# Kernel tuning notes

Hardware: AMD Instinct MI355X
Metric: run time of the kernel (lower is better)

## Reference

```python
import jax, jax.numpy as jnp
import numpy as np

B, T, IN, H, P = 1024, 100, 1, 256, 0.5


def _lstm_scan(xs, h0, c0, Wih, Whh, bih, bhh, mask_h, mask_in=None):
    """Run an LSTMCell over time with variational dropout masks.
    xs: [T, B, D]. mask_h multiplies the recurrent hidden state (as in the
    original: cell(x_t, (h * mask1, c))); mask_in (optional) multiplies input.
    PyTorch LSTMCell gate order: i, f, g, o."""
    b = bih + bhh

    def step(carry, xt):
        h, c = carry
        xin = xt if mask_in is None else xt * mask_in
        g = xin @ Wih.T + (h * mask_h) @ Whh.T + b  # [B, 4H]
        i, f, gg, o = jnp.split(g, 4, axis=-1)
        c = jax.nn.sigmoid(f) * c + jax.nn.sigmoid(i) * jnp.tanh(gg)
        h = jax.nn.sigmoid(o) * jnp.tanh(c)
        return (h, c), h

    _, hs = jax.lax.scan(step, (h0, c0), xs)
    return hs  # [T, B, H]


def setup_inputs() -> dict:
    key = jax.random.key(0)
    ks = jax.random.split(key, 24)
    s = 1.0 / np.sqrt(H)

    def u(k, shape):
        return jax.random.uniform(k, shape, jnp.float32, -s, s)

    inp = {"x0": jax.random.normal(ks[0], (B, T, IN), jnp.float32)}
    names = ["1f", "1b", "2f", "2b"]
    in_sizes = [2 * IN, 2 * IN, 2 * H, 2 * H]
    i = 1
    for n, d in zip(names, in_sizes):
        inp[f"Wih{n}"] = u(ks[i], (4 * H, d)); i += 1
        inp[f"Whh{n}"] = u(ks[i], (4 * H, H)); i += 1
        inp[f"bih{n}"] = u(ks[i], (4 * H,)); i += 1
        inp[f"bhh{n}"] = u(ks[i], (4 * H,)); i += 1
    inp["Wout"] = u(ks[17], (IN, 2 * H))
    inp["bout"] = u(ks[18], (IN,))
    # Variational dropout masks (Bernoulli(1 - dropout_prob)), per set_dropout(batch)
    def bern(k, shape):
        return (jax.random.uniform(k, shape) > P).astype(jnp.float32)
    inp["mask1"] = bern(ks[19], (B, H))
    inp["mask2"] = bern(ks[20], (B, 2 * H))
    inp["mask3"] = bern(ks[21], (B, H))
    inp["mask4"] = bern(ks[22], (B, 1, 2 * H))
    return inp


def reference(x0,
              Wih1f, Whh1f, bih1f, bhh1f,
              Wih1b, Whh1b, bih1b, bhh1b,
              Wih2f, Whh2f, bih2f, bhh2f,
              Wih2b, Whh2b, bih2b, bhh2b,
              Wout, bout, mask1, mask2, mask3, mask4):
    batch = x0.shape[0]
    m = x0.mean(axis=1, keepdims=True)                       # [B, 1, IN]
    x = jnp.concatenate([x0 - m, jnp.broadcast_to(m, x0.shape)], axis=2)  # [B, T, 2*IN]
    xs = jnp.swapaxes(x, 0, 1)                               # [T, B, 2*IN]

    h0 = jnp.zeros((batch, H), x0.dtype)
    c0 = jnp.zeros((batch, H), x0.dtype)

    # Layer 1, forward and backward in time (backward outputs NOT re-flipped,
    # faithful to the original which stacks them in reversed-visit order).
    hf = _lstm_scan(xs, h0, c0, Wih1f, Whh1f, bih1f, bhh1f, mask1)
    hb = _lstm_scan(xs[::-1], h0, c0, Wih1b, Whh1b, bih1b, bhh1b, mask1)
    p1 = jnp.concatenate([hf, hb], axis=-1)                  # [T, B, 2H]

    # Layer 2 with input mask2 and recurrent mask3
    h2f = _lstm_scan(p1, h0, c0, Wih2f, Whh2f, bih2f, bhh2f, mask3, mask_in=mask2)
    h2b = _lstm_scan(p1[::-1], h0, c0, Wih2b, Whh2b, bih2b, bhh2b, mask3, mask_in=mask2)
    p2 = jnp.concatenate([h2f, h2b], axis=-1)                # [T, B, 2H]

    pa = jnp.swapaxes(p2, 0, 1)                              # [B, T, 2H]
    pred = (pa * mask4) @ Wout.T + bout                      # [B, T, IN]
    return pred + m
```

## Files before the change

kernel.cpp:

```cpp
#include <hip/hip_runtime.h>
#include <cstdint>
#include <cstddef>

#define B_  1024
#define T_  100
#define H_  256

typedef _Float16 f16x8 __attribute__((ext_vector_type(8)));
typedef float    f32x16 __attribute__((ext_vector_type(16)));

__device__ __forceinline__ float sigm(float x){ return 1.0f/(1.0f + __expf(-x)); }
__device__ __forceinline__ float tanh_(float x){ return 1.0f - 2.0f/(1.0f + __expf(2.0f*x)); }

#define W_WHH1F 0
#define W_WHH1B 262144
#define W_WIH2F 524288
#define W_WIH2B 1048576
#define W_WHH2F 1572864
#define W_WHH2B 1835008
#define W_TOTAL 2097152

__global__ void pack_weights(const float* __restrict__ Whh1f, const float* __restrict__ Whh1b,
                             const float* __restrict__ Wih2f, const float* __restrict__ Wih2b,
                             const float* __restrict__ Whh2f, const float* __restrict__ Whh2b,
                             _Float16* __restrict__ dst)
{
  int fid = blockIdx.x*256 + threadIdx.x;
  const float* src; int base, nkk, ksh, lf;
  if      (fid <  32768){ src=Whh1f; base=W_WHH1F; nkk=16; ksh=4; lf=fid; }
  else if (fid <  65536){ src=Whh1b; base=W_WHH1B; nkk=16; ksh=4; lf=fid-32768; }
  else if (fid < 131072){ src=Wih2f; base=W_WIH2F; nkk=32; ksh=5; lf=fid-65536; }
  else if (fid < 196608){ src=Wih2b; base=W_WIH2B; nkk=32; ksh=5; lf=fid-131072; }
  else if (fid < 229376){ src=Whh2f; base=W_WHH2F; nkk=16; ksh=4; lf=fid-196608; }
  else                  { src=Whh2b; base=W_WHH2B; nkk=16; ksh=4; lf=fid-229376; }
  int l  = lf & 63;
  int t  = lf >> 6;
  int kk = t & (nkk-1);
  int r  = t >> ksh;
  int g  = r & 3, cc = r >> 2;
  int K  = nkk*16;
  int n  = g*256 + cc*32 + (l & 31);
  int k  = kk*16 + ((l >> 5) << 3);
  const float4* s4 = (const float4*)(src + (size_t)n*K + k);
  float4 v0 = s4[0], v1 = s4[1];
  f16x8 o;
  o[0]=(_Float16)v0.x; o[1]=(_Float16)v0.y; o[2]=(_Float16)v0.z; o[3]=(_Float16)v0.w;
  o[4]=(_Float16)v1.x; o[5]=(_Float16)v1.y; o[6]=(_Float16)v1.z; o[7]=(_Float16)v1.w;
  *(f16x8*)(dst + (size_t)base + (size_t)lf*8) = o;
}

__global__ __launch_bounds__(512, 2)
void l1_phase(const _Float16* __restrict__ wpool,
              const float* __restrict__ Wih_f, const float* __restrict__ Wih_b,
              const float* __restrict__ bih_f, const float* __restrict__ bhh_f,
              const float* __restrict__ bih_b, const float* __restrict__ bhh_b,
              const float* __restrict__ x0, const float* __restrict__ mvec,
              const float* __restrict__ mask1, const float* __restrict__ mask2,
              _Float16* __restrict__ p1m)
{
  __shared__ __align__(16) _Float16 hlds[8192];
  const int bid = blockIdx.x;
  const int dir = bid >> 5, rc = bid & 31;
  const int tid = threadIdx.x, lane = tid & 63, w = tid >> 6;
  const int b0 = rc*32;
  const int hcol = w*32 + (lane & 31);
  const _Float16* whh = wpool + (dir ? W_WHH1B : W_WHH1F);

  #pragma unroll
  for (int i = 0; i < 16; i++) hlds[tid + 512*i] = (_Float16)0.f;

  const float* Wih = dir ? Wih_b : Wih_f;
  const float* bih = dir ? bih_b : bih_f;
  const float* bhh = dir ? bhh_b : bhh_f;
  float wi0[4], wi1[4], bs[4];
  #pragma unroll
  for (int g = 0; g < 4; g++){
    int n = g*256 + hcol;
    wi0[g] = Wih[n*2]; wi1[g] = Wih[n*2 + 1];
    bs[g]  = bih[n] + bhh[n];
  }
  int rowv[16]; float m1v[16], m2v[16], mvv[16], creg[16];
  #pragma unroll
  for (int r = 0; r < 16; r++){
    int row = (r & 3) + 8*(r >> 2) + 4*(lane >> 5);
    rowv[r] = row;
    int b = b0 + row;
    m1v[r] = mask1[(size_t)b*H_ + hcol];
    m2v[r] = mask2[(size_t)b*512 + dir*256 + hcol];
    mvv[r] = mvec[b];
    creg[r] = 0.0f;
  }
  const int wbase = (hcol >> 4)*512 + ((hcol >> 3) & 1)*256 + (hcol & 7);
  __syncthreads();

  for (int s = 0; s < T_; s++){
    const int tin = dir ? (T_-1-s) : s;
    f32x16 acc[4];
    #pragma unroll
    for (int g = 0; g < 4; g++)
      #pragma unroll
      for (int e = 0; e < 16; e++) acc[g][e] = 0.0f;

    #pragma unroll 4
    for (int kk = 0; kk < 16; kk++){
      f16x8 a = *(const f16x8*)(hlds + kk*512 + lane*8);
      #pragma unroll
      for (int g = 0; g < 4; g++){
        f16x8 bw = *(const f16x8*)(whh + (size_t)(((w*4 + g)*16 + kk)*512 + lane*8));
        acc[g] = __builtin_amdgcn_mfma_f32_32x32x16_f16(a, bw, acc[g], 0, 0, 0);
      }
    }
    __syncthreads();

    #pragma unroll
    for (int r = 0; r < 16; r++){
      int b = b0 + rowv[r];
      float mv = mvv[r];
      float xd = x0[b*T_ + tin] - mv;
      float gi = acc[0][r] + xd*wi0[0] + mv*wi1[0] + bs[0];
      float gf = acc[1][r] + xd*wi0[1] + mv*wi1[1] + bs[1];
      float gg = acc[2][r] + xd*wi0[2] + mv*wi1[2] + bs[2];
      float go = acc[3][r] + xd*wi0[3] + mv*wi1[3] + bs[3];
      float ii = sigm(gi), ff = sigm(gf), g2 = tanh_(gg), oo = sigm(go);
      float cn = ff*creg[r] + ii*g2;
      creg[r] = cn;
      float h = oo*tanh_(cn);
      hlds[wbase + rowv[r]*8] = (_Float16)(h * m1v[r]);
      p1m[((size_t)s*B_ + b)*512 + dir*256 + hcol] = (_Float16)(h * m2v[r]);
    }
    __syncthreads();
  }
}

__global__ __launch_bounds__(512, 2)
void l2_phase(const _Float16* __restrict__ wpool,
              const float* __restrict__ bih_f, const float* __restrict__ bhh_f,
              const float* __restrict__ bih_b, const float* __restrict__ bhh_b,
              const _Float16* __restrict__ p1m,
              const float* __restrict__ mask3, const float* __restrict__ mask4,
              const float* __restrict__ Wout,
              float* __restrict__ pred)
{
  __shared__ __align__(16) _Float16 hlds[8192];
  const int bid = blockIdx.x;
  const int dir = bid >> 5, rc = bid & 31;
  const int tid = threadIdx.x, lane = tid & 63, w = tid >> 6;
  const int b0 = rc*32;
  const int hcol = w*32 + (lane & 31);
  const _Float16* whh = wpool + (dir ? W_WHH2B : W_WHH2F);
  const _Float16* wih = wpool + (dir ? W_WIH2B : W_WIH2F);

  #pragma unroll
  for (int i = 0; i < 16; i++) hlds[tid + 512*i] = (_Float16)0.f;

  const float* bih = dir ? bih_b : bih_f;
  const float* bhh = dir ? bhh_b : bhh_f;
  float bs[4];
  #pragma unroll
  for (int g = 0; g < 4; g++) bs[g] = bih[g*256 + hcol] + bhh[g*256 + hcol];
  float wo = Wout[dir*256 + hcol];
  int rowv[16]; float m3v[16], m4v[16], creg[16];
  #pragma unroll
  for (int r = 0; r < 16; r++){
    int row = (r & 3) + 8*(r >> 2) + 4*(lane >> 5);
    rowv[r] = row;
    int b = b0 + row;
    m3v[r] = mask3[(size_t)b*H_ + hcol];
    m4v[r] = mask4[(size_t)b*512 + dir*256 + hcol] * wo;
    creg[r] = 0.0f;
  }
  const int wbase = (hcol >> 4)*512 + ((hcol >> 3) & 1)*256 + (hcol & 7);
  __syncthreads();

  for (int s = 0; s < T_; s++){
    const int tin = dir ? (T_-1-s) : s;
    f32x16 acc[4];
    #pragma unroll
    for (int g = 0; g < 4; g++)
      #pragma unroll
      for (int e = 0; e < 16; e++) acc[g][e] = 0.0f;

    #pragma unroll 4
    for (int kk = 0; kk < 16; kk++){
      f16x8 a = *(const f16x8*)(hlds + kk*512 + lane*8);
      #pragma unroll
      for (int g = 0; g < 4; g++){
        f16x8 bw = *(const f16x8*)(whh + (size_t)(((w*4 + g)*16 + kk)*512 + lane*8));
        acc[g] = __builtin_amdgcn_mfma_f32_32x32x16_f16(a, bw, acc[g], 0, 0, 0);
      }
    }
    const _Float16* arow2 = p1m + ((size_t)tin*B_ + b0 + (lane & 31))*512 + ((lane >> 5) << 3);
    #pragma unroll 4
    for (int kk = 0; kk < 32; kk++){
      f16x8 a = *(const f16x8*)(arow2 + kk*16);
      #pragma unroll
      for (int g = 0; g < 4; g++){
        f16x8 bw = *(const f16x8*)(wih + (size_t)(((w*4 + g)*32 + kk)*512 + lane*8));
        acc[g] = __builtin_amdgcn_mfma_f32_32x32x16_f16(a, bw, acc[g], 0, 0, 0);
      }
    }
    __syncthreads();

    #pragma unroll
    for (int r = 0; r < 16; r++){
      int b = b0 + rowv[r];
      float gi = acc[0][r] + bs[0];
      float gf = acc[1][r] + bs[1];
      float gg = acc[2][r] + bs[2];
      float go = acc[3][r] + bs[3];
      float ii = sigm(gi), ff = sigm(gf), g2 = tanh_(gg), oo = sigm(go);
      float cn = ff*creg[r] + ii*g2;
      creg[r] = cn;
      float h = oo*tanh_(cn);
      hlds[wbase + rowv[r]*8] = (_Float16)(h * m3v[r]);
      float contrib = h * m4v[r];
      contrib += __shfl_xor(contrib, 16);
      contrib += __shfl_xor(contrib, 8);
      contrib += __shfl_xor(contrib, 4);
      contrib += __shfl_xor(contrib, 2);
      contrib += __shfl_xor(contrib, 1);
      if ((lane & 31) == 0) atomicAdd(&pred[(size_t)b*T_ + s], contrib);
    }
    __syncthreads();
  }
}

__global__ void prep_kernel(const float* __restrict__ x0, float* __restrict__ mvec)
{
  int b = blockIdx.x*blockDim.x + threadIdx.x;
  if (b < B_){
    float ssum = 0.0f;
    for (int t = 0; t < T_; t++) ssum += x0[b*T_ + t];
    mvec[b] = ssum * (1.0f / T_);
  }
}

__global__ void final_kernel(const float* __restrict__ pred,
                             const float* __restrict__ mvec,
                             const float* __restrict__ bout,
                             float* __restrict__ out)
{
  int idx = blockIdx.x*256 + threadIdx.x;
  if (idx < B_*T_){
    int b = idx / T_;
    out[idx] = pred[idx] + bout[0] + mvec[b];
  }
}

extern "C" void kernel_launch(void* const* d_in, const int* in_sizes, int n_in,
                              void* d_out, int out_size, void* d_ws, size_t ws_size,
                              hipStream_t stream)
{
  (void)in_sizes; (void)n_in; (void)out_size; (void)ws_size;
  const float* x0    = (const float*)d_in[0];
  const float* Wih1f = (const float*)d_in[1];
  const float* Whh1f = (const float*)d_in[2];
  const float* bih1f = (const float*)d_in[3];
  const float* bhh1f = (const float*)d_in[4];
  const float* Wih1b = (const float*)d_in[5];
  const float* Whh1b = (const float*)d_in[6];
  const float* bih1b = (const float*)d_in[7];
  const float* bhh1b = (const float*)d_in[8];
  const float* Wih2f = (const float*)d_in[9];
  const float* Whh2f = (const float*)d_in[10];
  const float* bih2f = (const float*)d_in[11];
  const float* bhh2f = (const float*)d_in[12];
  const float* Wih2b = (const float*)d_in[13];
  const float* Whh2b = (const float*)d_in[14];
  const float* bih2b = (const float*)d_in[15];
  const float* bhh2b = (const float*)d_in[16];
  const float* Wout  = (const float*)d_in[17];
  const float* bout  = (const float*)d_in[18];
  const float* mask1 = (const float*)d_in[19];
  const float* mask2 = (const float*)d_in[20];
  const float* mask3 = (const float*)d_in[21];
  const float* mask4 = (const float*)d_in[22];
  float* out = (float*)d_out;

  char* ws = (char*)d_ws;
  size_t off = 0;
  _Float16* wpool = (_Float16*)(ws + off); off += (size_t)W_TOTAL*2;
  _Float16* p1m   = (_Float16*)(ws + off); off += (size_t)T_*B_*512*2;
  float* pred = (float*)(ws + off); off += (size_t)B_*T_*4;
  float* mvec = (float*)(ws + off); off += 4096;

  hipMemsetAsync(pred, 0, (size_t)B_*T_*4, stream);

  pack_weights<<<dim3(1024), dim3(256), 0, stream>>>(
      Whh1f, Whh1b, Wih2f, Wih2b, Whh2f, Whh2b, wpool);
  prep_kernel<<<dim3(4), dim3(256), 0, stream>>>(x0, mvec);

  l1_phase<<<dim3(64), dim3(512), 0, stream>>>(wpool, Wih1f, Wih1b,
      bih1f, bhh1f, bih1b, bhh1b, x0, mvec, mask1, mask2, p1m);
  l2_phase<<<dim3(64), dim3(512), 0, stream>>>(wpool, bih2f, bhh2f,
      bih2b, bhh2b, p1m, mask3, mask4, Wout, pred);
  final_kernel<<<dim3((B_*T_ + 255)/256), dim3(256), 0, stream>>>(pred, mvec, bout, out);
}
```

Before: 6.003 ms.

## Software-pipeline MFMA operand loads and remap blocks by direction across XCDs

The inner MFMA loops in both LSTM phases now use a 4-deep register ring that prefetches the A fragments (from LDS or p1m) and the B weight fragments ahead of their use. Layer 2's two K loops are merged into a single 48-step stream so the prefetch runs across the boundary. Block indices are remapped so each group of 8 consecutive blocks mixes both directions, which is intended to spread each direction's weight traffic across XCDs and their L2 caches. x0 is also pre-transposed to [T,B] so per-step input reads are coalesced, and launch bounds drop to 1 block per SM so the prefetch buffers have register room. The cost is higher register pressure and one extra small transpose kernel.

```diff
diff --git a/kernel.cpp b/kernel.cpp
--- a/kernel.cpp
+++ b/kernel.cpp
@@ -49,22 +49,24 @@
   *(f16x8*)(dst + (size_t)base + (size_t)lf*8) = o;
 }
 
-__global__ __launch_bounds__(512, 2)
+__global__ __launch_bounds__(512, 1)
 void l1_phase(const _Float16* __restrict__ wpool,
               const float* __restrict__ Wih_f, const float* __restrict__ Wih_b,
               const float* __restrict__ bih_f, const float* __restrict__ bhh_f,
               const float* __restrict__ bih_b, const float* __restrict__ bhh_b,
-              const float* __restrict__ x0, const float* __restrict__ mvec,
+              const float* __restrict__ xT, const float* __restrict__ mvec,
               const float* __restrict__ mask1, const float* __restrict__ mask2,
               _Float16* __restrict__ p1m)
 {
   __shared__ __align__(16) _Float16 hlds[8192];
   const int bid = blockIdx.x;
-  const int dir = bid >> 5, rc = bid & 31;
+  const int xm = bid & 7;
+  const int dir = xm >> 2;
+  const int rc  = ((bid >> 3) << 2) | (xm & 3);
   const int tid = threadIdx.x, lane = tid & 63, w = tid >> 6;
   const int b0 = rc*32;
   const int hcol = w*32 + (lane & 31);
-  const _Float16* whh = wpool + (dir ? W_WHH1B : W_WHH1F);
+  const _Float16* whhW = wpool + (dir ? W_WHH1B : W_WHH1F) + (size_t)(w*4)*16*512 + lane*8;
 
   #pragma unroll
   for (int i = 0; i < 16; i++) hlds[tid + 512*i] = (_Float16)0.f;
@@ -101,14 +103,29 @@
       #pragma unroll
       for (int e = 0; e < 16; e++) acc[g][e] = 0.0f;
 
-    #pragma unroll 4
+    f16x8 bq[4][4], aq[4];
+    #pragma unroll
+    for (int p = 0; p < 4; p++){
+      aq[p] = *(const f16x8*)(hlds + p*512 + lane*8);
+      #pragma unroll
+      for (int g = 0; g < 4; g++)
+        bq[p][g] = *(const f16x8*)(whhW + (size_t)(g*16 + p)*512);
+    }
+    #pragma unroll
     for (int kk = 0; kk < 16; kk++){
-      f16x8 a = *(const f16x8*)(hlds + kk*512 + lane*8);
-      #pragma unroll
-      for (int g = 0; g < 4; g++){
-        f16x8 bw = *(const f16x8*)(whh + (size_t)(((w*4 + g)*16 + kk)*512 + lane*8));
-        acc[g] = __builtin_amdgcn_mfma_f32_32x32x16_f16(a, bw, acc[g], 0, 0, 0);
+      const int slot = kk & 3;
+      f16x8 a  = aq[slot];
+      f16x8 w0 = bq[slot][0], w1 = bq[slot][1], w2 = bq[slot][2], w3 = bq[slot][3];
+      if (kk + 4 < 16){
+        aq[slot] = *(const f16x8*)(hlds + (kk+4)*512 + lane*8);
+        #pragma unroll
+        for (int g = 0; g < 4; g++)
+          bq[slot][g] = *(const f16x8*)(whhW + (size_t)(g*16 + kk + 4)*512);
       }
+      acc[0] = __builtin_amdgcn_mfma_f32_32x32x16_f16(a, w0, acc[0], 0, 0, 0);
+      acc[1] = __builtin_amdgcn_mfma_f32_32x32x16_f16(a, w1, acc[1], 0, 0, 0);
+      acc[2] = __builtin_amdgcn_mfma_f32_32x32x16_f16(a, w2, acc[2], 0, 0, 0);
+      acc[3] = __builtin_amdgcn_mfma_f32_32x32x16_f16(a, w3, acc[3], 0, 0, 0);
     }
     __syncthreads();
 
@@ -116,7 +133,7 @@
     for (int r = 0; r < 16; r++){
       int b = b0 + rowv[r];
       float mv = mvv[r];
-      float xd = x0[b*T_ + tin] - mv;
+      float xd = xT[tin*B_ + b] - mv;
       float gi = acc[0][r] + xd*wi0[0] + mv*wi1[0] + bs[0];
       float gf = acc[1][r] + xd*wi0[1] + mv*wi1[1] + bs[1];
       float gg = acc[2][r] + xd*wi0[2] + mv*wi1[2] + bs[2];
@@ -132,7 +149,7 @@
   }
 }
 
-__global__ __launch_bounds__(512, 2)
+__global__ __launch_bounds__(512, 1)
 void l2_phase(const _Float16* __restrict__ wpool,
               const float* __restrict__ bih_f, const float* __restrict__ bhh_f,
               const float* __restrict__ bih_b, const float* __restrict__ bhh_b,
@@ -143,12 +160,14 @@
 {
   __shared__ __align__(16) _Float16 hlds[8192];
   const int bid = blockIdx.x;
-  const int dir = bid >> 5, rc = bid & 31;
+  const int xm = bid & 7;
+  const int dir = xm >> 2;
+  const int rc  = ((bid >> 3) << 2) | (xm & 3);
   const int tid = threadIdx.x, lane = tid & 63, w = tid >> 6;
   const int b0 = rc*32;
   const int hcol = w*32 + (lane & 31);
-  const _Float16* whh = wpool + (dir ? W_WHH2B : W_WHH2F);
-  const _Float16* wih = wpool + (dir ? W_WIH2B : W_WIH2F);
+  const _Float16* whhW = wpool + (dir ? W_WHH2B : W_WHH2F) + (size_t)(w*4)*16*512 + lane*8;
+  const _Float16* wihW = wpool + (dir ? W_WIH2B : W_WIH2F) + (size_t)(w*4)*32*512 + lane*8;
 
   #pragma unroll
   for (int i = 0; i < 16; i++) hlds[tid + 512*i] = (_Float16)0.f;
@@ -174,31 +193,43 @@
 
   for (int s = 0; s < T_; s++){
     const int tin = dir ? (T_-1-s) : s;
+    const _Float16* arow2 = p1m + ((size_t)tin*B_ + b0 + (lane & 31))*512 + ((lane >> 5) << 3);
+
     f32x16 acc[4];
     #pragma unroll
     for (int g = 0; g < 4; g++)
       #pragma unroll
       for (int e = 0; e < 16; e++) acc[g][e] = 0.0f;
 
-    #pragma unroll 4
-    for (int kk = 0; kk < 16; kk++){
-      f16x8 a = *(const f16x8*)(hlds + kk*512 + lane*8);
+    #define A_FRAG(vs) ((vs) < 16 ? *(const f16x8*)(hlds + (vs)*512 + lane*8) \
+                                  : *(const f16x8*)(arow2 + ((vs)-16)*16))
+    #define B_FRAG(vs, g) ((vs) < 16 ? *(const f16x8*)(whhW + (size_t)((g)*16 + (vs))*512) \
+                                     : *(const f16x8*)(wihW + (size_t)((g)*32 + ((vs)-16))*512))
+
+    f16x8 bq[4][4], aq[4];
+    #pragma unroll
+    for (int p = 0; p < 4; p++){
+      aq[p] = A_FRAG(p);
       #pragma unroll
-      for (int g = 0; g < 4; g++){
-        f16x8 bw = *(const f16x8*)(whh + (size_t)(((w*4 + g)*16 + kk)*512 + lane*8));
-        acc[g] = __builtin_amdgcn_mfma_f32_32x32x16_f16(a, bw, acc[g], 0, 0, 0);
+      for (int g = 0; g < 4; g++) bq[p][g] = B_FRAG(p, g);
+    }
+    #pragma unroll
+    for (int vs = 0; vs < 48; vs++){
+      const int slot = vs & 3;
+      f16x8 a  = aq[slot];
+      f16x8 w0 = bq[slot][0], w1 = bq[slot][1], w2 = bq[slot][2], w3 = bq[slot][3];
+      if (vs + 4 < 48){
+        aq[slot] = A_FRAG(vs + 4);
+        #pragma unroll
+        for (int g = 0; g < 4; g++) bq[slot][g] = B_FRAG(vs + 4, g);
       }
-    }
-    const _Float16* arow2 = p1m + ((size_t)tin*B_ + b0 + (lane & 31))*512 + ((lane >> 5) << 3);
-    #pragma unroll 4
-    for (int kk = 0; kk < 32; kk++){
-      f16x8 a = *(const f16x8*)(arow2 + kk*16);
-      #pragma unroll
-      for (int g = 0; g < 4; g++){
-        f16x8 bw = *(const f16x8*)(wih + (size_t)(((w*4 + g)*32 + kk)*512 + lane*8));
-        acc[g] = __builtin_amdgcn_mfma_f32_32x32x16_f16(a, bw, acc[g], 0, 0, 0);
-      }
-    }
+      acc[0] = __builtin_amdgcn_mfma_f32_32x32x16_f16(a, w0, acc[0], 0, 0, 0);
+      acc[1] = __builtin_amdgcn_mfma_f32_32x32x16_f16(a, w1, acc[1], 0, 0, 0);
+      acc[2] = __builtin_amdgcn_mfma_f32_32x32x16_f16(a, w2, acc[2], 0, 0, 0);
+      acc[3] = __builtin_amdgcn_mfma_f32_32x32x16_f16(a, w3, acc[3], 0, 0, 0);
+    }
+    #undef A_FRAG
+    #undef B_FRAG
     __syncthreads();
 
     #pragma unroll
@@ -232,6 +263,16 @@
     float ssum = 0.0f;
     for (int t = 0; t < T_; t++) ssum += x0[b*T_ + t];
     mvec[b] = ssum * (1.0f / T_);
+  }
+}
+
+__global__ void prep2_kernel(const float* __restrict__ x0, float* __restrict__ xT)
+{
+  int idx = blockIdx.x*256 + threadIdx.x;
+  if (idx < B_*T_){
+    int t = idx >> 10;
+    int b = idx & 1023;
+    xT[idx] = x0[b*T_ + t];
   }
 }
 
@@ -282,6 +323,7 @@
   _Float16* wpool = (_Float16*)(ws + off); off += (size_t)W_TOTAL*2;
   _Float16* p1m   = (_Float16*)(ws + off); off += (size_t)T_*B_*512*2;
   float* pred = (float*)(ws + off); off += (size_t)B_*T_*4;
+  float* xT   = (float*)(ws + off); off += (size_t)B_*T_*4;
   float* mvec = (float*)(ws + off); off += 4096;
 
   hipMemsetAsync(pred, 0, (size_t)B_*T_*4, stream);
@@ -289,9 +331,10 @@
   pack_weights<<<dim3(1024), dim3(256), 0, stream>>>(
       Whh1f, Whh1b, Wih2f, Wih2b, Whh2f, Whh2b, wpool);
   prep_kernel<<<dim3(4), dim3(256), 0, stream>>>(x0, mvec);
+  prep2_kernel<<<dim3((B_*T_ + 255)/256), dim3(256), 0, stream>>>(x0, xT);
 
   l1_phase<<<dim3(64), dim3(512), 0, stream>>>(wpool, Wih1f, Wih1b,
-      bih1f, bhh1f, bih1b, bhh1b, x0, mvec, mask1, mask2, p1m);
+      bih1f, bhh1f, bih1b, bhh1b, xT, mvec, mask1, mask2, p1m);
   l2_phase<<<dim3(64), dim3(512), 0, stream>>>(wpool, bih2f, bhh2f,
       bih2b, bhh2b, p1m, mask3, mask4, Wout, pred);
   final_kernel<<<dim3((B_*T_ + 255)/256), dim3(256), 0, stream>>>(pred, mvec, bout, out);
```

New measurement: 9.718 ms. +61.9%, slower.
